# Kernel tuning notes

Hardware: AMD Instinct MI355X
Metric: run time of the kernel (lower is better)

The kernel has to match this reference:

```python
import jax, jax.numpy as jnp
import numpy as np

N = 8192
D_IN, D_MID, D_EMB = 1024, 256, 64
N_EDGES = N * 8


def setup_inputs() -> dict:
    key = jax.random.key(0)
    ks = jax.random.split(key, 6)
    X = jax.random.normal(ks[0], (N, D_IN), dtype=jnp.float32)
    # Xavier-uniform style init as in get_weight_initial
    b1 = np.sqrt(6.0 / (D_IN + D_MID))
    b2 = np.sqrt(6.0 / (D_MID + D_EMB))
    W1 = jax.random.uniform(ks[1], (D_IN, D_MID), minval=-b1, maxval=b1, dtype=jnp.float32)
    W2 = jax.random.uniform(ks[2], (D_MID, D_EMB), minval=-b2, maxval=b2, dtype=jnp.float32)
    edge_val = jax.random.uniform(ks[3], (N_EDGES,), dtype=jnp.float32)
    edge_src = jax.random.randint(ks[4], (N_EDGES,), 0, N, dtype=jnp.int32)
    edge_dst = jax.random.randint(ks[5], (N_EDGES,), 0, N, dtype=jnp.int32)
    return {"X": X, "W1": W1, "W2": W2, "edge_val": edge_val,
            "edge_src": edge_src, "edge_dst": edge_dst}


def reference(X, W1, W2, edge_val, edge_src, edge_dst):
    n = X.shape[0]

    def spmm(H):  # sparse Laplacian (COO) times dense H
        return jax.ops.segment_sum(edge_val[:, None] * H[edge_src], edge_dst,
                                   num_segments=n)

    h = jax.nn.relu(spmm(X @ W1))          # [N, D_MID]
    emb = spmm(h @ W2)                      # [N, D_EMB]
    # pairwise squared Euclidean distances between rows of emb -> [N, N]
    sq = jnp.sum(emb * emb, axis=1)
    dist = sq[:, None] + sq[None, :] - 2.0 * (emb @ emb.T)
    recons_w = jax.nn.softmax(-dist, axis=1) + 1e-10
    return recons_w
```

## Files before the change

### kernel.cpp

```cpp
#include <hip/hip_runtime.h>
#include <cstddef>

constexpr int NN    = 8192;
constexpr int DIN   = 1024;
constexpr int DMID  = 256;
constexpr int DEMB  = 64;
constexpr int NEDGE = 65536;

typedef __attribute__((ext_vector_type(8))) short bf16x8;
typedef __attribute__((ext_vector_type(4))) float f32x4;
#define MFMA16(a, b, c) __builtin_amdgcn_mfma_f32_16x16x32_bf16((a), (b), (c), 0, 0, 0)

__device__ __forceinline__ unsigned short bf16_rne(float x) {
  unsigned u = __float_as_uint(x);
  return (unsigned short)((u + 0x7FFFu + ((u >> 16) & 1u)) >> 16);
}
__device__ __forceinline__ float bf16_tof(unsigned short h) {
  return __uint_as_float((unsigned)h << 16);
}

__global__ __launch_bounds__(256) void wconv_kernel(const float* __restrict__ W1,
                                                    const float* __restrict__ W2,
                                                    unsigned short* __restrict__ W1b,
                                                    unsigned short* __restrict__ W2b)
{
  int idx = blockIdx.x * 256 + threadIdx.x;
  if (idx < DMID * DIN) {
    int n = idx >> 10, k = idx & 1023;
    W1b[idx] = bf16_rne(W1[k * DMID + n]);
  } else {
    int t = idx - DMID * DIN;
    int n = t >> 8, k = t & 255;
    W2b[t] = bf16_rne(W2[k * DEMB + n]);
  }
}

__global__ __launch_bounds__(256) void hist_kernel(const int* __restrict__ dst,
                                                   int* __restrict__ counts)
{
  int e = blockIdx.x * 256 + threadIdx.x;
  atomicAdd(&counts[dst[e]], 1);
}

__global__ __launch_bounds__(256) void scan_kernel(const int* __restrict__ counts,
                                                   int* __restrict__ row_start)
{
  __shared__ int sums[256];
  const int t = threadIdx.x;
  int local[32];
  int s = 0;
#pragma unroll
  for (int i = 0; i < 32; ++i) { local[i] = counts[t * 32 + i]; s += local[i]; }
  sums[t] = s;
  __syncthreads();
  for (int off = 1; off < 256; off <<= 1) {
    int v = (t >= off) ? sums[t - off] : 0;
    __syncthreads();
    sums[t] += v;
    __syncthreads();
  }
  int base = (t == 0) ? 0 : sums[t - 1];
#pragma unroll
  for (int i = 0; i < 32; ++i) { row_start[t * 32 + i] = base; base += local[i]; }
  if (t == 255) row_start[NN] = base;
}

__global__ __launch_bounds__(256) void scatter_kernel(
    const int* __restrict__ src, const float* __restrict__ val,
    const int* __restrict__ dst, const int* __restrict__ row_start,
    int* __restrict__ cursor, int* __restrict__ csr_src, float* __restrict__ csr_val)
{
  int e = blockIdx.x * 256 + threadIdx.x;
  int d = dst[e];
  int pos = row_start[d] + atomicAdd(&cursor[d], 1);
  csr_src[pos] = src[e];
  csr_val[pos] = val[e];
}

__global__ __launch_bounds__(256) void gemm1_kernel(
    const float* __restrict__ X, const unsigned short* __restrict__ W1b,
    float* __restrict__ H1)
{
  const int lane = threadIdx.x & 63;
  const int wave = threadIdx.x >> 6;
  const int m0 = blockIdx.y * 64 + wave * 16;
  const int n0 = blockIdx.x * 64;
  const int rl = lane & 15;
  const int kq = (lane >> 4) * 8;
  f32x4 zero = {0.f, 0.f, 0.f, 0.f};
  f32x4 acc[4] = {zero, zero, zero, zero};
  for (int s = 0; s < DIN / 32; ++s) {
    const int kb = s * 32 + kq;
    const float* xp = X + (size_t)(m0 + rl) * DIN + kb;
    float4 x0 = *(const float4*)xp;
    float4 x1 = *(const float4*)(xp + 4);
    bf16x8 ah;
    ah[0] = (short)bf16_rne(x0.x); ah[1] = (short)bf16_rne(x0.y);
    ah[2] = (short)bf16_rne(x0.z); ah[3] = (short)bf16_rne(x0.w);
    ah[4] = (short)bf16_rne(x1.x); ah[5] = (short)bf16_rne(x1.y);
    ah[6] = (short)bf16_rne(x1.z); ah[7] = (short)bf16_rne(x1.w);
#pragma unroll
    for (int ns = 0; ns < 4; ++ns) {
      bf16x8 bh = *(const bf16x8*)(W1b + (size_t)(n0 + ns * 16 + rl) * DIN + kb);
      acc[ns] = MFMA16(ah, bh, acc[ns]);
    }
  }
  const int rq = (lane >> 4) * 4;
#pragma unroll
  for (int ns = 0; ns < 4; ++ns)
#pragma unroll
    for (int r = 0; r < 4; ++r)
      H1[(size_t)(m0 + rq + r) * DMID + n0 + ns * 16 + rl] = acc[ns][r];
}

__global__ __launch_bounds__(256) void spmm1_kernel(
    const float* __restrict__ H, const int* __restrict__ row_start,
    const int* __restrict__ csr_src, const float* __restrict__ csr_val,
    unsigned short* __restrict__ Hb)
{
  const int lane = threadIdx.x & 63;
  const int wave = threadIdx.x >> 6;
  const int r = blockIdx.x * 4 + wave;
  const int e0 = row_start[r];
  const int e1 = row_start[r + 1];
  const int c = lane * 4;
  float4 acc = make_float4(0.f, 0.f, 0.f, 0.f);
  for (int e = e0; e < e1; ++e) {
    const int s   = csr_src[e];
    const float v = csr_val[e];
    float4 h = *(const float4*)(H + (size_t)s * DMID + c);
    acc.x = fmaf(v, h.x, acc.x);
    acc.y = fmaf(v, h.y, acc.y);
    acc.z = fmaf(v, h.z, acc.z);
    acc.w = fmaf(v, h.w, acc.w);
  }
  ushort4 h;
  h.x = bf16_rne(fmaxf(acc.x, 0.f));
  h.y = bf16_rne(fmaxf(acc.y, 0.f));
  h.z = bf16_rne(fmaxf(acc.z, 0.f));
  h.w = bf16_rne(fmaxf(acc.w, 0.f));
  *(ushort4*)(Hb + (size_t)r * DMID + c) = h;
}

__global__ __launch_bounds__(256) void gemm2_kernel(
    const unsigned short* __restrict__ Ab, const unsigned short* __restrict__ W2b,
    float* __restrict__ E1)
{
  const int lane = threadIdx.x & 63;
  const int wave = threadIdx.x >> 6;
  const int m0 = blockIdx.x * 64 + wave * 16;
  const int rl = lane & 15;
  const int kq = (lane >> 4) * 8;
  f32x4 zero = {0.f, 0.f, 0.f, 0.f};
  f32x4 acc[4] = {zero, zero, zero, zero};
  for (int s = 0; s < DMID / 32; ++s) {
    const int kb = s * 32 + kq;
    bf16x8 ah = *(const bf16x8*)(Ab + (size_t)(m0 + rl) * DMID + kb);
#pragma unroll
    for (int ns = 0; ns < 4; ++ns) {
      bf16x8 bh = *(const bf16x8*)(W2b + (size_t)(ns * 16 + rl) * DMID + kb);
      acc[ns] = MFMA16(ah, bh, acc[ns]);
    }
  }
  const int rq = (lane >> 4) * 4;
#pragma unroll
  for (int ns = 0; ns < 4; ++ns)
#pragma unroll
    for (int r = 0; r < 4; ++r)
      E1[(size_t)(m0 + rq + r) * DEMB + ns * 16 + rl] = acc[ns][r];
}

__global__ __launch_bounds__(256) void spmm2_kernel(
    const float* __restrict__ H, const int* __restrict__ row_start,
    const int* __restrict__ csr_src, const float* __restrict__ csr_val,
    unsigned short* __restrict__ EmbH, float* __restrict__ sqv)
{
  const int lane = threadIdx.x & 63;
  const int wave = threadIdx.x >> 6;
  const int r = blockIdx.x * 4 + wave;
  const int e0 = row_start[r];
  const int e1 = row_start[r + 1];
  float acc = 0.f;
  for (int e = e0; e < e1; ++e)
    acc = fmaf(csr_val[e], H[(size_t)csr_src[e] * DEMB + lane], acc);
  unsigned short h = bf16_rne(acc);
  EmbH[(size_t)r * DEMB + lane] = h;
  float hf = bf16_tof(h);
  float sq = hf * hf;
#pragma unroll
  for (int off = 32; off; off >>= 1) sq += __shfl_xor(sq, off, 64);
  if (lane == 0) sqv[r] = sq;
}

__device__ __forceinline__ void dist_tile_hh(
    const unsigned short* __restrict__ EH, int ibase, int jbase, int lane,
    f32x4 (&acc)[4][4])
{
  const int rl = lane & 15;
  const int kq = (lane >> 4) * 8;
#pragma unroll
  for (int s = 0; s < 2; ++s) {
    const int kb = s * 32 + kq;
    bf16x8 a[4], b[4];
#pragma unroll
    for (int t = 0; t < 4; ++t) {
      a[t] = *(const bf16x8*)(EH + (size_t)(ibase + t * 16 + rl) * DEMB + kb);
      b[t] = *(const bf16x8*)(EH + (size_t)(jbase + t * 16 + rl) * DEMB + kb);
    }
#pragma unroll
    for (int ms = 0; ms < 4; ++ms)
#pragma unroll
      for (int ns = 0; ns < 4; ++ns)
        acc[ms][ns] = MFMA16(a[ms], b[ns], acc[ms][ns]);
  }
}

__global__ __launch_bounds__(256) void rowsum_sym_kernel(
    const unsigned short* __restrict__ EH, const float* __restrict__ sq,
    float* __restrict__ rowsum)
{
  const int bi = blockIdx.y, bj = blockIdx.x;
  if (bj < bi) return;
  const int lane = threadIdx.x & 63;
  const int wave = threadIdx.x >> 6;
  const int wr = wave >> 1, wc = wave & 1;
  const int ibase = bi * 128 + wr * 64;
  const int jbase = bj * 128 + wc * 64;
  const int rl = lane & 15;
  const int rq = (lane >> 4) * 4;

  f32x4 zero = {0.f, 0.f, 0.f, 0.f};
  f32x4 acc[4][4];
#pragma unroll
  for (int ms = 0; ms < 4; ++ms)
#pragma unroll
    for (int ns = 0; ns < 4; ++ns) acc[ms][ns] = zero;
  dist_tile_hh(EH, ibase, jbase, lane, acc);

  float si[4][4], sj[4];
#pragma unroll
  for (int ms = 0; ms < 4; ++ms)
#pragma unroll
    for (int r = 0; r < 4; ++r) si[ms][r] = sq[ibase + ms * 16 + rq + r];
#pragma unroll
  for (int ns = 0; ns < 4; ++ns) sj[ns] = sq[jbase + ns * 16 + rl];

  float rs[4][4] = {};
  float cs[4]    = {};
#pragma unroll
  for (int ms = 0; ms < 4; ++ms)
#pragma unroll
    for (int ns = 0; ns < 4; ++ns)
#pragma unroll
      for (int r = 0; r < 4; ++r) {
        float v = __expf(fmaf(2.f, acc[ms][ns][r], -si[ms][r] - sj[ns]));
        rs[ms][r] += v;
        cs[ns]    += v;
      }

#pragma unroll
  for (int ms = 0; ms < 4; ++ms)
#pragma unroll
    for (int r = 0; r < 4; ++r) {
      float v = rs[ms][r];
      v += __shfl_xor(v, 1, 64);
      v += __shfl_xor(v, 2, 64);
      v += __shfl_xor(v, 4, 64);
      v += __shfl_xor(v, 8, 64);
      if (rl == 0) atomicAdd(&rowsum[ibase + ms * 16 + rq + r], v);
    }

  if (bi != bj) {
#pragma unroll
    for (int ns = 0; ns < 4; ++ns) {
      float v = cs[ns];
      v += __shfl_xor(v, 16, 64);
      v += __shfl_xor(v, 32, 64);
      if (lane < 16) atomicAdd(&rowsum[jbase + ns * 16 + rl], v);
    }
  }
}

__global__ __launch_bounds__(256) void dist_write_kernel(
    const unsigned short* __restrict__ EH, const float* __restrict__ sq,
    const float* __restrict__ rowsum, float* __restrict__ out)
{
  const int lane = threadIdx.x & 63;
  const int wave = threadIdx.x >> 6;
  const int wr = wave >> 1, wc = wave & 1;
  const int ibase = blockIdx.y * 128 + wr * 64;
  const int jbase = blockIdx.x * 128 + wc * 64;
  const int rl = lane & 15;
  const int rq = (lane >> 4) * 4;

  f32x4 zero = {0.f, 0.f, 0.f, 0.f};
  f32x4 acc[4][4];
#pragma unroll
  for (int ms = 0; ms < 4; ++ms)
#pragma unroll
    for (int ns = 0; ns < 4; ++ns) acc[ms][ns] = zero;
  dist_tile_hh(EH, ibase, jbase, lane, acc);

  float si[4][4], ri[4][4], sj[4];
#pragma unroll
  for (int ms = 0; ms < 4; ++ms)
#pragma unroll
    for (int r = 0; r < 4; ++r) {
      const int i = ibase + ms * 16 + rq + r;
      si[ms][r] = sq[i];
      ri[ms][r] = 1.f / rowsum[i];
    }
#pragma unroll
  for (int ns = 0; ns < 4; ++ns) sj[ns] = sq[jbase + ns * 16 + rl];

#pragma unroll
  for (int ms = 0; ms < 4; ++ms)
#pragma unroll
    for (int r = 0; r < 4; ++r) {
      const size_t row = (size_t)(ibase + ms * 16 + rq + r) * NN;
#pragma unroll
      for (int ns = 0; ns < 4; ++ns) {
        float e = __expf(fmaf(2.f, acc[ms][ns][r], -si[ms][r] - sj[ns]));
        out[row + jbase + ns * 16 + rl] = fmaf(e, ri[ms][r], 1e-10f);
      }
    }
}

extern "C" void kernel_launch(void* const* d_in, const int* in_sizes, int n_in,
                              void* d_out, int out_size, void* d_ws, size_t ws_size,
                              hipStream_t stream)
{
  const float* X  = (const float*)d_in[0];
  const float* W1 = (const float*)d_in[1];
  const float* W2 = (const float*)d_in[2];
  const float* ev = (const float*)d_in[3];
  const int* esrc = (const int*)d_in[4];
  const int* edst = (const int*)d_in[5];
  float* out = (float*)d_out;

  char* p = (char*)d_ws;
  auto alloc = [&](size_t bytes) { char* q = p; p += (bytes + 255) & ~(size_t)255; return q; };

  int*   counts    = (int*)alloc(NN * 4);
  int*   cursor    = (int*)alloc(NN * 4);
  float* rowsum    = (float*)alloc(NN * 4);
  int*   row_start = (int*)alloc((NN + 1) * 4);
  int*   csr_src   = (int*)alloc(NEDGE * 4);
  float* csr_val   = (float*)alloc(NEDGE * 4);
  float* sqv       = (float*)alloc(NN * 4);
  float* H1        = (float*)alloc((size_t)NN * DMID * 4);
  float* E1        = (float*)alloc((size_t)NN * DEMB * 4);
  unsigned short* W1b  = (unsigned short*)alloc((size_t)DMID * DIN * 2);
  unsigned short* W2b  = (unsigned short*)alloc((size_t)DEMB * DMID * 2);
  unsigned short* H1b  = (unsigned short*)alloc((size_t)NN * DMID * 2);
  unsigned short* EmbH = (unsigned short*)alloc((size_t)NN * DEMB * 2);

  hipMemsetAsync(d_ws, 0, (size_t)3 * NN * 4, stream);

  wconv_kernel<<<(DMID * DIN + DEMB * DMID) / 256, 256, 0, stream>>>(W1, W2, W1b, W2b);
  hist_kernel<<<NEDGE / 256, 256, 0, stream>>>(edst, counts);
  scan_kernel<<<1, 256, 0, stream>>>(counts, row_start);
  scatter_kernel<<<NEDGE / 256, 256, 0, stream>>>(esrc, ev, edst, row_start, cursor,
                                                  csr_src, csr_val);

  gemm1_kernel<<<dim3(DMID / 64, NN / 64), 256, 0, stream>>>(X, W1b, H1);
  spmm1_kernel<<<NN / 4, 256, 0, stream>>>(H1, row_start, csr_src, csr_val, H1b);
  gemm2_kernel<<<NN / 64, 256, 0, stream>>>(H1b, W2b, E1);
  spmm2_kernel<<<NN / 4, 256, 0, stream>>>(E1, row_start, csr_src, csr_val, EmbH, sqv);

  rowsum_sym_kernel<<<dim3(NN / 128, NN / 128), 256, 0, stream>>>(EmbH, sqv, rowsum);
  dist_write_kernel<<<dim3(NN / 128, NN / 128), 256, 0, stream>>>(EmbH, sqv, rowsum, out);
}
```

Measured before the change: 463.9 us.

## Widen gemm1 to full N per block, store bf16 intermediate, fuse prep kernels

Each gemm1 block now computes all 256 output columns, so every X row is read and converted to bf16 once instead of four times. The gemm1 output is stored as bf16, which halves the write traffic and the gather traffic in spmm1. The weight-conversion and histogram kernels are merged into one launch. The costs are more accumulator registers (16 f32x4 per lane), fewer blocks (128) and so less parallelism across the GPU, plus an extra bf16 rounding on the intermediate.

```diff
diff --git a/kernel.cpp b/kernel.cpp
--- a/kernel.cpp
+++ b/kernel.cpp
@@ -19,27 +19,29 @@
   return __uint_as_float((unsigned)h << 16);
 }
 
-__global__ __launch_bounds__(256) void wconv_kernel(const float* __restrict__ W1,
-                                                    const float* __restrict__ W2,
-                                                    unsigned short* __restrict__ W1b,
-                                                    unsigned short* __restrict__ W2b)
-{
-  int idx = blockIdx.x * 256 + threadIdx.x;
-  if (idx < DMID * DIN) {
-    int n = idx >> 10, k = idx & 1023;
-    W1b[idx] = bf16_rne(W1[k * DMID + n]);
+constexpr int WCONV_BLOCKS = (DMID * DIN + DEMB * DMID) / 256;
+__global__ __launch_bounds__(256) void prep_kernel(const float* __restrict__ W1,
+                                                   const float* __restrict__ W2,
+                                                   unsigned short* __restrict__ W1b,
+                                                   unsigned short* __restrict__ W2b,
+                                                   const int* __restrict__ edst,
+                                                   int* __restrict__ counts)
+{
+  int b = blockIdx.x;
+  if (b < WCONV_BLOCKS) {
+    int idx = b * 256 + threadIdx.x;
+    if (idx < DMID * DIN) {
+      int n = idx >> 10, k = idx & 1023;
+      W1b[idx] = bf16_rne(W1[k * DMID + n]);
+    } else {
+      int t = idx - DMID * DIN;
+      int n = t >> 8, k = t & 255;
+      W2b[t] = bf16_rne(W2[k * DEMB + n]);
+    }
   } else {
-    int t = idx - DMID * DIN;
-    int n = t >> 8, k = t & 255;
-    W2b[t] = bf16_rne(W2[k * DEMB + n]);
-  }
-}
-
-__global__ __launch_bounds__(256) void hist_kernel(const int* __restrict__ dst,
-                                                   int* __restrict__ counts)
-{
-  int e = blockIdx.x * 256 + threadIdx.x;
-  atomicAdd(&counts[dst[e]], 1);
+    int e = (b - WCONV_BLOCKS) * 256 + threadIdx.x;
+    atomicAdd(&counts[edst[e]], 1);
+  }
 }
 
 __global__ __launch_bounds__(256) void scan_kernel(const int* __restrict__ counts,
@@ -79,16 +81,18 @@
 
 __global__ __launch_bounds__(256) void gemm1_kernel(
     const float* __restrict__ X, const unsigned short* __restrict__ W1b,
-    float* __restrict__ H1)
-{
-  const int lane = threadIdx.x & 63;
-  const int wave = threadIdx.x >> 6;
-  const int m0 = blockIdx.y * 64 + wave * 16;
-  const int n0 = blockIdx.x * 64;
+    unsigned short* __restrict__ G1)
+{
+  const int lane = threadIdx.x & 63;
+  const int wave = threadIdx.x >> 6;
+  const int m0 = blockIdx.x * 64 + wave * 16;
   const int rl = lane & 15;
   const int kq = (lane >> 4) * 8;
   f32x4 zero = {0.f, 0.f, 0.f, 0.f};
-  f32x4 acc[4] = {zero, zero, zero, zero};
+  f32x4 acc[16];
+#pragma unroll
+  for (int ns = 0; ns < 16; ++ns) acc[ns] = zero;
+
   for (int s = 0; s < DIN / 32; ++s) {
     const int kb = s * 32 + kq;
     const float* xp = X + (size_t)(m0 + rl) * DIN + kb;
@@ -100,21 +104,21 @@
     ah[4] = (short)bf16_rne(x1.x); ah[5] = (short)bf16_rne(x1.y);
     ah[6] = (short)bf16_rne(x1.z); ah[7] = (short)bf16_rne(x1.w);
 #pragma unroll
-    for (int ns = 0; ns < 4; ++ns) {
-      bf16x8 bh = *(const bf16x8*)(W1b + (size_t)(n0 + ns * 16 + rl) * DIN + kb);
+    for (int ns = 0; ns < 16; ++ns) {
+      bf16x8 bh = *(const bf16x8*)(W1b + (size_t)(ns * 16 + rl) * DIN + kb);
       acc[ns] = MFMA16(ah, bh, acc[ns]);
     }
   }
   const int rq = (lane >> 4) * 4;
 #pragma unroll
-  for (int ns = 0; ns < 4; ++ns)
+  for (int ns = 0; ns < 16; ++ns)
 #pragma unroll
     for (int r = 0; r < 4; ++r)
-      H1[(size_t)(m0 + rq + r) * DMID + n0 + ns * 16 + rl] = acc[ns][r];
+      G1[(size_t)(m0 + rq + r) * DMID + ns * 16 + rl] = bf16_rne(acc[ns][r]);
 }
 
 __global__ __launch_bounds__(256) void spmm1_kernel(
-    const float* __restrict__ H, const int* __restrict__ row_start,
+    const unsigned short* __restrict__ G1, const int* __restrict__ row_start,
     const int* __restrict__ csr_src, const float* __restrict__ csr_val,
     unsigned short* __restrict__ Hb)
 {
@@ -128,11 +132,11 @@
   for (int e = e0; e < e1; ++e) {
     const int s   = csr_src[e];
     const float v = csr_val[e];
-    float4 h = *(const float4*)(H + (size_t)s * DMID + c);
-    acc.x = fmaf(v, h.x, acc.x);
-    acc.y = fmaf(v, h.y, acc.y);
-    acc.z = fmaf(v, h.z, acc.z);
-    acc.w = fmaf(v, h.w, acc.w);
+    ushort4 h = *(const ushort4*)(G1 + (size_t)s * DMID + c);
+    acc.x = fmaf(v, bf16_tof(h.x), acc.x);
+    acc.y = fmaf(v, bf16_tof(h.y), acc.y);
+    acc.z = fmaf(v, bf16_tof(h.z), acc.z);
+    acc.w = fmaf(v, bf16_tof(h.w), acc.w);
   }
   ushort4 h;
   h.x = bf16_rne(fmaxf(acc.x, 0.f));
@@ -348,23 +352,22 @@
   int*   csr_src   = (int*)alloc(NEDGE * 4);
   float* csr_val   = (float*)alloc(NEDGE * 4);
   float* sqv       = (float*)alloc(NN * 4);
-  float* H1        = (float*)alloc((size_t)NN * DMID * 4);
   float* E1        = (float*)alloc((size_t)NN * DEMB * 4);
   unsigned short* W1b  = (unsigned short*)alloc((size_t)DMID * DIN * 2);
   unsigned short* W2b  = (unsigned short*)alloc((size_t)DEMB * DMID * 2);
+  unsigned short* G1   = (unsigned short*)alloc((size_t)NN * DMID * 2);
   unsigned short* H1b  = (unsigned short*)alloc((size_t)NN * DMID * 2);
   unsigned short* EmbH = (unsigned short*)alloc((size_t)NN * DEMB * 2);
 
   hipMemsetAsync(d_ws, 0, (size_t)3 * NN * 4, stream);
 
-  wconv_kernel<<<(DMID * DIN + DEMB * DMID) / 256, 256, 0, stream>>>(W1, W2, W1b, W2b);
-  hist_kernel<<<NEDGE / 256, 256, 0, stream>>>(edst, counts);
+  prep_kernel<<<WCONV_BLOCKS + NEDGE / 256, 256, 0, stream>>>(W1, W2, W1b, W2b, edst, counts);
   scan_kernel<<<1, 256, 0, stream>>>(counts, row_start);
   scatter_kernel<<<NEDGE / 256, 256, 0, stream>>>(esrc, ev, edst, row_start, cursor,
                                                   csr_src, csr_val);
 
-  gemm1_kernel<<<dim3(DMID / 64, NN / 64), 256, 0, stream>>>(X, W1b, H1);
-  spmm1_kernel<<<NN / 4, 256, 0, stream>>>(H1, row_start, csr_src, csr_val, H1b);
+  gemm1_kernel<<<NN / 64, 256, 0, stream>>>(X, W1b, G1);
+  spmm1_kernel<<<NN / 4, 256, 0, stream>>>(G1, row_start, csr_src, csr_val, H1b);
   gemm2_kernel<<<NN / 64, 256, 0, stream>>>(H1b, W2b, E1);
   spmm2_kernel<<<NN / 4, 256, 0, stream>>>(E1, row_start, csr_src, csr_val, EmbH, sqv);
 
```

Result: slower. 530.7 us (+14.4%).
